# Kernel tuning notes

Measured on AMD Instinct MI355X. Metric: run time of the kernel, lower is better.

The kernel has to match this reference:

```python
import jax
jax.config.update("jax_enable_x64", True)
import jax.numpy as jnp
import numpy as np

CKA_WEIGHT = 0.1


def _group_cka_sum(feats):
    """feats: [F, N, D] float. Returns sum of pairwise CKA over all (i,j) pairs.

    Faithful to CKASR: K = X X^T with zeroed diagonal, unbiased HSIC
    (Song et al. estimator), CKA[i,j] = HSIC(Ki,Kj)/sqrt(HSIC(Ki,Ki)HSIC(Kj,Kj)).
    All pairwise loops are batched into einsums.
    """
    F, N, D = feats.shape
    X = feats.reshape(F, N, D).astype(jnp.float64)
    K = jnp.einsum('fnd,fmd->fnm', X, X)                 # [F,N,N] Gram
    K = K * (1.0 - jnp.eye(N, dtype=K.dtype))            # fill_diagonal_(0)
    # HSIC(Ki, Kj) = 1/(N(N-3)) * ( tr(Ki Kj)
    #   + sum(Ki) sum(Kj) / ((N-1)(N-2))
    #   - 2/(N-2) * <rowsum(Ki), rowsum(Kj)> )
    trKL = jnp.einsum('iab,jab->ij', K, K)               # tr(Ki Kj), K symmetric
    s = jnp.sum(K, axis=(1, 2))                          # [F] total sums
    r = jnp.sum(K, axis=2)                               # [F,N] row sums
    rr = jnp.einsum('ia,ja->ij', r, r)                   # [F,F]
    hsic = (trKL + jnp.outer(s, s) / ((N - 1) * (N - 2))
            - 2.0 * rr / (N - 2)) / (N * (N - 3))        # [F,F]
    d = jnp.sqrt(jnp.diagonal(hsic))                     # [F]
    cka = hsic / (d[:, None] * d[None, :])
    return jnp.sum(cka)


def setup_inputs() -> dict:
    key = jax.random.key(0)
    k1, k2, k3, k4 = jax.random.split(key, 4)
    N, C = 64, 1000
    output = jax.random.normal(k1, (N, C), dtype=jnp.float32)
    target = jax.random.randint(k2, (N,), 0, C, dtype=jnp.int64)
    feats_a = jax.random.normal(k3, (3, N, 65536), dtype=jnp.float32)
    feats_b = jax.random.normal(k4, (4, N, 32768), dtype=jnp.float32)
    return {"output": output, "target": target,
            "feats_a": feats_a, "feats_b": feats_b}


def reference(output, target, feats_a, feats_b):
    N = output.shape[0]
    logp = jax.nn.log_softmax(output.astype(jnp.float32), axis=-1)
    ce = -jnp.mean(logp[jnp.arange(N), target])           # CrossEntropyLoss (mean)
    cka = _group_cka_sum(feats_a) + _group_cka_sum(feats_b)
    loss = ce + CKA_WEIGHT * cka.astype(jnp.float32)
    return (loss, output)
```

## Files before the change

kernel.cpp:

```cpp
#include <hip/hip_runtime.h>
#include <hip/hip_bf16.h>
#include <math.h>

typedef __attribute__((ext_vector_type(8))) short short8;
typedef __attribute__((ext_vector_type(4))) float f32x4;

#define PSTRIDE 4160

__device__ __forceinline__ unsigned int bf16_rn(float x) {
    unsigned int u = __float_as_uint(x);
    return (u + 0x7FFFu + ((u >> 16) & 1u)) >> 16;
}

__global__ __launch_bounds__(256) void ce_kernel(
    const float* __restrict__ logits, const int* __restrict__ target,
    float* __restrict__ out_copy, float* __restrict__ ce_rows)
{
    const int row = blockIdx.x;
    const float* x = logits + row * 1000;
    const int t = threadIdx.x;
    __shared__ float red[256];

    float m = -INFINITY;
    for (int i = t; i < 1000; i += 256) {
        float v = x[i];
        out_copy[row * 1000 + i] = v;
        m = fmaxf(m, v);
    }
    red[t] = m; __syncthreads();
    for (int s = 128; s > 0; s >>= 1) {
        if (t < s) red[t] = fmaxf(red[t], red[t + s]);
        __syncthreads();
    }
    m = red[0];
    __syncthreads();

    float ssum = 0.f;
    for (int i = t; i < 1000; i += 256) ssum += expf(x[i] - m);
    red[t] = ssum; __syncthreads();
    for (int s = 128; s > 0; s >>= 1) {
        if (t < s) red[t] += red[t + s];
        __syncthreads();
    }
    if (t == 0) {
        double lse = (double)m + log((double)red[0]);
        int tg = target[row];
        ce_rows[row] = (float)(-((double)x[tg] - lse));
    }
}

__global__ __launch_bounds__(256) void gramf_kernel(
    const float* __restrict__ A, const float* __restrict__ B,
    float* __restrict__ partials, int nfA, int nfB)
{
    __shared__ f32x4 ldsv[4096];
    char* lds = (char*)ldsv;

    const int blk = blockIdx.x;
    const int uA = nfA * 128;
    const float* xf;
    int c, D;
    if (blk < uA) {
        int f = blk >> 7; c = blk & 127; D = 65536;
        xf = A + (size_t)f * 64 * 65536;
    } else {
        int v = blk - uA;
        int f = v >> 6; c = v & 63; D = 32768;
        xf = B + (size_t)f * 64 * 32768;
    }

    const int t = threadIdx.x;
    const int wave = t >> 6, lane = t & 63;
    const int k0 = c * 512;

#pragma unroll 4
    for (int rr = 0; rr < 16; ++rr) {
        const int row = wave * 16 + rr;
        const float* p = xf + (size_t)row * D + k0 + lane * 8;
        float4 va = *(const float4*)p;
        float4 vb = *(const float4*)(p + 4);
        float vv[8] = {va.x, va.y, va.z, va.w, vb.x, vb.y, vb.z, vb.w};
        short8 hv;
#pragma unroll
        for (int j = 0; j < 8; ++j) hv[j] = (short)bf16_rn(vv[j]);
        const int boff = (lane * 16) ^ ((row & 7) << 4);
        *(short8*)(lds + row * 1024 + boff) = hv;
    }
    __syncthreads();

    const int m = lane & 15, quad = lane >> 4;
    const int loff = wave * 256 + quad * 16;

    f32x4 acc[4][4];
#pragma unroll
    for (int i = 0; i < 4; ++i)
#pragma unroll
        for (int j = 0; j < 4; ++j) acc[i][j] = (f32x4)0.f;

    short8 fr[4][4];
#pragma unroll
    for (int s = 0; s < 4; ++s)
#pragma unroll
        for (int tm = 0; tm < 4; ++tm) {
            const int row = tm * 16 + m;
            const int boff = (loff + s * 64) ^ ((row & 7) << 4);
            fr[s][tm] = *(const short8*)(lds + row * 1024 + boff);
        }
#pragma unroll
    for (int s = 0; s < 4; ++s)
#pragma unroll
        for (int tm = 0; tm < 4; ++tm)
#pragma unroll
            for (int tn = 0; tn < 4; ++tn)
                acc[tm][tn] = __builtin_amdgcn_mfma_f32_16x16x32_bf16(
                    fr[s][tm], fr[s][tn], acc[tm][tn], 0, 0, 0);

    __syncthreads();
    float* kbuf = (float*)lds;
    if (wave == 0) {
#pragma unroll
        for (int tm = 0; tm < 4; ++tm)
#pragma unroll
            for (int tn = 0; tn < 4; ++tn)
#pragma unroll
                for (int r = 0; r < 4; ++r)
                    kbuf[(tm * 16 + quad * 4 + r) * 64 + tn * 16 + m] = acc[tm][tn][r];
    }
    __syncthreads();
    if (wave != 0) {
#pragma unroll
        for (int tm = 0; tm < 4; ++tm)
#pragma unroll
            for (int tn = 0; tn < 4; ++tn)
#pragma unroll
                for (int r = 0; r < 4; ++r)
                    atomicAdd(&kbuf[(tm * 16 + quad * 4 + r) * 64 + tn * 16 + m],
                              acc[tm][tn][r]);
    }
    __syncthreads();

    float4* outp = (float4*)(partials + (size_t)blk * PSTRIDE);
    const float4* kb4 = (const float4*)kbuf;
    for (int e = t; e < 1024; e += 256) outp[e] = kb4[e];
}

__global__ __launch_bounds__(256) void reduce_kernel(
    const float* __restrict__ partials, float* __restrict__ K, int singleF)
{
    __shared__ double red[256];
    int f, eblk, base, count;
    if (singleF < 0) {
        f = blockIdx.x >> 6; eblk = blockIdx.x & 63;
        if (f < 3) { base = f * 128;            count = 128; }
        else       { base = 384 + (f - 3) * 64; count = 64;  }
    } else {
        f = singleF; eblk = blockIdx.x; base = 0;
        count = (f < 3) ? 128 : 64;
    }
    const int e = (eblk << 6) + (threadIdx.x & 63);
    const int jg = threadIdx.x >> 6;

    double s0 = 0.0, s1 = 0.0;
    for (int j = jg; j < count; j += 8) {
        s0 += (double)partials[(size_t)(base + j) * PSTRIDE + e];
        s1 += (double)partials[(size_t)(base + j + 4) * PSTRIDE + e];
    }
    red[threadIdx.x] = s0 + s1;
    __syncthreads();
    if (jg == 0) {
        double tot = red[threadIdx.x] + red[threadIdx.x + 64]
                   + red[threadIdx.x + 128] + red[threadIdx.x + 192];
        int rr = e >> 6, cc = e & 63;
        K[f * 4096 + e] = (rr == cc) ? 0.f : (float)tot;
    }
}

__global__ __launch_bounds__(256) void hsic_kernel(
    const float* __restrict__ K, double* __restrict__ hsic_out)
{
    const int p = blockIdx.x;
    int i, j;
    if (p < 9) { i = p / 3; j = p % 3; }
    else       { int q = p - 9; i = 3 + q / 4; j = 3 + q % 4; }
    const float* Ki = K + i * 4096;
    const float* Kj = K + j * 4096;
    const int t = threadIdx.x;

    __shared__ double red[256];
    __shared__ double ri[64], rj[64];

    double local = 0.0;
    for (int e = t; e < 4096; e += 256)
        local += (double)Ki[e] * (double)Kj[e];
    red[t] = local; __syncthreads();
    for (int s = 128; s > 0; s >>= 1) {
        if (t < s) red[t] += red[t + s];
        __syncthreads();
    }

    if (t < 64) {
        double s = 0.0;
        for (int mc = 0; mc < 64; ++mc) s += (double)Ki[t * 64 + mc];
        ri[t] = s;
    } else if (t < 128) {
        int n = t - 64;
        double s = 0.0;
        for (int mc = 0; mc < 64; ++mc) s += (double)Kj[n * 64 + mc];
        rj[n] = s;
    }
    __syncthreads();

    if (t == 0) {
        double tr = red[0];
        double rr = 0.0, si = 0.0, sj = 0.0;
        for (int n = 0; n < 64; ++n) {
            rr += ri[n] * rj[n];
            si += ri[n];
            sj += rj[n];
        }
        const double N = 64.0;
        const double c1 = (N - 1.0) * (N - 2.0);
        const double c2 = N - 2.0;
        const double c3 = N * (N - 3.0);
        hsic_out[p] = (tr + si * sj / c1 - 2.0 * rr / c2) / c3;
    }
}

__global__ __launch_bounds__(64) void final_kernel(
    const double* __restrict__ hsic, const float* __restrict__ ce_rows,
    float* __restrict__ out_loss)
{
    if (threadIdx.x != 0) return;
    double ce = 0.0;
    for (int n = 0; n < 64; ++n) ce += (double)ce_rows[n];
    ce /= 64.0;

    double cka_total = 0.0;
    for (int i = 0; i < 3; ++i)
        for (int j = 0; j < 3; ++j)
            cka_total += hsic[i * 3 + j] / sqrt(hsic[i * 3 + i] * hsic[j * 3 + j]);
    for (int i = 0; i < 4; ++i)
        for (int j = 0; j < 4; ++j)
            cka_total += hsic[9 + i * 4 + j] / sqrt(hsic[9 + i * 4 + i] * hsic[9 + j * 4 + j]);

    out_loss[0] = (float)(ce + 0.1 * cka_total);
}

extern "C" void kernel_launch(void* const* d_in, const int* in_sizes, int n_in,
                              void* d_out, int out_size, void* d_ws, size_t ws_size,
                              hipStream_t stream)
{
    const float* output  = (const float*)d_in[0];
    const int*   target  = (const int*)d_in[1];
    const float* feats_a = (const float*)d_in[2];
    const float* feats_b = (const float*)d_in[3];
    float* out = (float*)d_out;

    char* ws = (char*)d_ws;
    float*  K       = (float*)ws;
    float*  ce_rows = (float*)(ws + 114688);
    double* hsic    = (double*)(ws + 114944);
    float*  partials = (float*)(ws + 131072);

    const size_t partMain = (size_t)640 * PSTRIDE * 4;
    const size_t mainNeed = 131072 + partMain;

    hipLaunchKernelGGL(ce_kernel, dim3(64), dim3(256), 0, stream,
                       output, target, out + 1, ce_rows);

    if (ws_size >= mainNeed) {
        hipLaunchKernelGGL(gramf_kernel, dim3(640), dim3(256), 0, stream,
                           feats_a, feats_b, partials, 3, 4);
        hipLaunchKernelGGL(reduce_kernel, dim3(448), dim3(256), 0, stream,
                           partials, K, -1);
    } else {
        for (int f = 0; f < 7; ++f) {
            if (f < 3) {
                const float* X = feats_a + (size_t)f * 64 * 65536;
                hipLaunchKernelGGL(gramf_kernel, dim3(128), dim3(256), 0, stream,
                                   X, (const float*)nullptr, partials, 1, 0);
            } else {
                const float* X = feats_b + (size_t)(f - 3) * 64 * 32768;
                hipLaunchKernelGGL(gramf_kernel, dim3(64), dim3(256), 0, stream,
                                   (const float*)nullptr, X, partials, 0, 1);
            }
            hipLaunchKernelGGL(reduce_kernel, dim3(64), dim3(256), 0, stream,
                               partials, K, f);
        }
    }

    hipLaunchKernelGGL(hsic_kernel, dim3(25), dim3(256), 0, stream, K, hsic);
    hipLaunchKernelGGL(final_kernel, dim3(1), dim3(64), 0, stream,
                       hsic, ce_rows, out);
}
```

Before: 182.1 us.

## Load Gram input tiles directly into LDS via global_load_lds in two halves

Replaces the register-staged global load and bf16 conversion before the LDS write with direct global-to-LDS DMA loads of fp32 data, done in two 256-column halves with a swizzled layout. The bf16 rounding now happens after reading from LDS, just before the MFMA. The aim is to cut register pressure and VGPR round trips on the load path and issue loads more efficiently. In exchange, LDS traffic doubles because fp32 is stored, the conversion work is repeated per fragment, and an extra barrier splits the two halves.

```diff
diff --git a/kernel.cpp b/kernel.cpp
--- a/kernel.cpp
+++ b/kernel.cpp
@@ -53,9 +53,7 @@
     const float* __restrict__ A, const float* __restrict__ B,
     float* __restrict__ partials, int nfA, int nfB)
 {
-    __shared__ f32x4 ldsv[4096];
-    char* lds = (char*)ldsv;
-
+    __shared__ float lbuf[16384];
     const int blk = blockIdx.x;
     const int uA = nfA * 128;
     const float* xf;
@@ -71,25 +69,7 @@
 
     const int t = threadIdx.x;
     const int wave = t >> 6, lane = t & 63;
-    const int k0 = c * 512;
-
-#pragma unroll 4
-    for (int rr = 0; rr < 16; ++rr) {
-        const int row = wave * 16 + rr;
-        const float* p = xf + (size_t)row * D + k0 + lane * 8;
-        float4 va = *(const float4*)p;
-        float4 vb = *(const float4*)(p + 4);
-        float vv[8] = {va.x, va.y, va.z, va.w, vb.x, vb.y, vb.z, vb.w};
-        short8 hv;
-#pragma unroll
-        for (int j = 0; j < 8; ++j) hv[j] = (short)bf16_rn(vv[j]);
-        const int boff = (lane * 16) ^ ((row & 7) << 4);
-        *(short8*)(lds + row * 1024 + boff) = hv;
-    }
-    __syncthreads();
-
     const int m = lane & 15, quad = lane >> 4;
-    const int loff = wave * 256 + quad * 16;
 
     f32x4 acc[4][4];
 #pragma unroll
@@ -97,26 +77,52 @@
 #pragma unroll
         for (int j = 0; j < 4; ++j) acc[i][j] = (f32x4)0.f;
 
-    short8 fr[4][4];
-#pragma unroll
-    for (int s = 0; s < 4; ++s)
-#pragma unroll
-        for (int tm = 0; tm < 4; ++tm) {
-            const int row = tm * 16 + m;
-            const int boff = (loff + s * 64) ^ ((row & 7) << 4);
-            fr[s][tm] = *(const short8*)(lds + row * 1024 + boff);
+    for (int h = 0; h < 2; ++h) {
+        const int k0 = c * 512 + h * 256;
+        if (h) __syncthreads();
+
+#pragma unroll
+        for (int rr = 0; rr < 16; ++rr) {
+            const int row = wave * 16 + rr;
+            const int gb = (lane * 16) ^ ((row & 7) << 4);
+            const float* src = xf + (size_t)row * D + k0 + (gb >> 2);
+            __builtin_amdgcn_global_load_lds(
+                (const __attribute__((address_space(1))) void*)src,
+                (__attribute__((address_space(3))) void*)&lbuf[row * 256],
+                16, 0, 0);
         }
-#pragma unroll
-    for (int s = 0; s < 4; ++s)
-#pragma unroll
-        for (int tm = 0; tm < 4; ++tm)
-#pragma unroll
-            for (int tn = 0; tn < 4; ++tn)
-                acc[tm][tn] = __builtin_amdgcn_mfma_f32_16x16x32_bf16(
-                    fr[s][tm], fr[s][tn], acc[tm][tn], 0, 0, 0);
-
-    __syncthreads();
-    float* kbuf = (float*)lds;
+        asm volatile("s_waitcnt vmcnt(0)" ::: "memory");
+        __syncthreads();
+
+#pragma unroll
+        for (int s = 0; s < 2; ++s) {
+            short8 fr[4];
+#pragma unroll
+            for (int tt = 0; tt < 4; ++tt) {
+                const int row = tt * 16 + m;
+                const int col = (wave * 64 + s * 32 + quad * 8) * 4;
+                const int sw = (row & 7) << 4;
+                const char* rb = (const char*)&lbuf[row * 256];
+                float4 a = *(const float4*)(rb + (col ^ sw));
+                float4 b = *(const float4*)(rb + ((col + 16) ^ sw));
+                short8 hv;
+                hv[0] = (short)bf16_rn(a.x); hv[1] = (short)bf16_rn(a.y);
+                hv[2] = (short)bf16_rn(a.z); hv[3] = (short)bf16_rn(a.w);
+                hv[4] = (short)bf16_rn(b.x); hv[5] = (short)bf16_rn(b.y);
+                hv[6] = (short)bf16_rn(b.z); hv[7] = (short)bf16_rn(b.w);
+                fr[tt] = hv;
+            }
+#pragma unroll
+            for (int tm = 0; tm < 4; ++tm)
+#pragma unroll
+                for (int tn = 0; tn < 4; ++tn)
+                    acc[tm][tn] = __builtin_amdgcn_mfma_f32_16x16x32_bf16(
+                        fr[tm], fr[tn], acc[tm][tn], 0, 0, 0);
+        }
+    }
+
+    __syncthreads();
+    float* kbuf = (float*)lbuf;
     if (wave == 0) {
 #pragma unroll
         for (int tm = 0; tm < 4; ++tm)
```

Measured after the change: 179.3 us. Within noise of the previous version (-1.5%).
